# Kernel optimization log

Measured on AMD Instinct MI355X. Metric: run time of the kernel, lower is better.

Reference implementation:

```python
import jax, jax.numpy as jnp
import numpy as np

BONE_NUM = 16
THRESH = 0.7


def masked_l2(out, tar, mask):
    # out, tar: [B, C, H, W]; mask: [B, H, W]
    diff_norm = jnp.linalg.norm(out - tar, axis=1)          # [B, H, W]
    masked = jnp.where(mask > THRESH, diff_norm, 0.0)
    B = out.shape[0]
    flat_m = masked.reshape(B, -1)
    flat_d = diff_norm.reshape(B, -1)
    cnt = jnp.sum(flat_m != 0, axis=1)                       # device-side nonzero count
    per_sample = jnp.where(
        cnt > 0,
        flat_m.sum(axis=1) / jnp.maximum(cnt, 1).astype(flat_m.dtype),
        flat_d.mean(axis=1),
    )
    return per_sample.mean()


def pose_nocs_loss(pred_joint_map, pred_joint_score, out_mask, tar_joints):
    # pred_joint_map: [B, bn*3, H, W]; pred_joint_score: [B, bn, H, W]
    # out_mask: [B, H, W]; tar_joints: [B, bn, 3]
    B, _, H, W = pred_joint_map.shape
    bn = BONE_NUM
    jm = pred_joint_map.reshape(B, bn, 3, H, W) * out_mask[:, None, None]
    score = jax.nn.sigmoid(pred_joint_score) * out_mask[:, None]        # [B, bn, H, W]
    denom = score.reshape(B, bn, -1).sum(axis=2)[:, :, None, None] + 1e-5
    score_map = score / denom
    jm = jax.lax.stop_gradient(jm) * score_map[:, :, None]              # [B, bn, 3, H, W]
    pred_joint = jm.reshape(B, bn, 3, -1).sum(axis=3)                   # [B, bn, 3]
    loss = jnp.linalg.norm(pred_joint - tar_joints, axis=2).sum()
    return loss / (B * bn)


def setup_inputs() -> dict:
    key = jax.random.key(0)
    k1, k2, k3 = jax.random.split(key, 3)
    B, H, W = 4, 256, 256
    bn = BONE_NUM
    output = jax.random.normal(k1, (B, 4 + bn * 8 + 2, H, W), dtype=jnp.float32)
    tar_maps = jax.random.uniform(k2, (B, 4 + bn * 6 + 1, H, W), dtype=jnp.float32)
    tar_pose = jax.random.normal(k3, (B, bn, 6), dtype=jnp.float32)
    return {"output": output, "tar_maps": tar_maps, "tar_pose": tar_pose}


def reference(output, tar_maps, tar_pose):
    bn = BONE_NUM
    B = output.shape[0]

    # --- slice predictions ---
    pred_nocs = output[:, 0:3]
    mask_logits = output[:, 3]                                # sigmoid applied below
    pred_loc_map = jax.nn.sigmoid(output[:, 4:4 + bn * 3])
    pred_rot_map = jax.nn.sigmoid(output[:, 4 + bn * 3:4 + bn * 6])
    pred_skin_seg = output[:, 4 + bn * 6:4 + bn * 7 + 2]       # [B, bn+2, H, W]
    pred_joint_score = output[:, 4 + bn * 7 + 2:4 + bn * 8 + 2]  # [B, bn, H, W]

    # --- slice targets ---
    target_nocs = tar_maps[:, 0:3]
    target_mask = tar_maps[:, 3]
    tar_loc_map = jax.nn.sigmoid(tar_maps[:, 4:4 + bn * 3])
    tar_rot_map = jax.nn.sigmoid(tar_maps[:, 4 + bn * 3:4 + bn * 6])
    tar_skin_seg = tar_maps[:, 4 + bn * 6].astype(jnp.int32)   # [B, H, W]
    tar_loc = jax.nn.sigmoid(tar_pose[:, :, 0:3])
    tar_rot = jax.nn.sigmoid(tar_pose[:, :, 3:6])

    # --- BCE mask loss (on sigmoid(mask_logits) vs target_mask), stable form ---
    mask_loss = -jnp.mean(
        target_mask * jax.nn.log_sigmoid(mask_logits)
        + (1.0 - target_mask) * jax.nn.log_sigmoid(-mask_logits)
    )

    # --- masked L2 losses ---
    nocs_loss = masked_l2(pred_nocs, target_nocs, target_mask)
    loc_map_loss = masked_l2(pred_loc_map, tar_loc_map, target_mask)
    rot_map_loss = masked_l2(pred_rot_map, tar_rot_map, target_mask)

    # --- skinning cross entropy ---
    logits = jnp.transpose(pred_skin_seg, (0, 2, 3, 1)).reshape(-1, bn + 2)
    labels = tar_skin_seg.reshape(-1)
    logp = jax.nn.log_softmax(logits, axis=-1)
    skin_loss = -jnp.mean(jnp.take_along_axis(logp, labels[:, None], axis=1))

    # --- pose losses ---
    loc_loss = pose_nocs_loss(pred_loc_map, pred_joint_score, target_mask, tar_loc)
    rot_loss = pose_nocs_loss(pred_rot_map, pred_joint_score, target_mask, tar_rot)

    return jnp.stack([nocs_loss, mask_loss, loc_loss, loc_map_loss,
                      rot_loss, rot_map_loss, skin_loss])
```

## Files before the change

### kernel.cpp

```cpp
#include <hip/hip_runtime.h>
#include <math.h>

#define HW 65536
#define BN 16


__device__ __forceinline__ float fsig(float x) {
    return __builtin_amdgcn_rcpf(1.0f + __expf(-x));
}
__device__ __forceinline__ float sq(float x) { return x * x; }

__device__ __forceinline__ float wred(float v) {
#pragma unroll
    for (int off = 32; off; off >>= 1) v += __shfl_xor(v, off, 64);
    return v;
}

__global__ __launch_bounds__(256) void mvpm_pix2(const float* __restrict__ outp,
                                                 const float* __restrict__ tarp,
                                                 float* __restrict__ ws) {
    const int b = blockIdx.y;
    const int t = blockIdx.x * 256 + threadIdx.x;
    const int C2 = HW / 2;
    const float2* ob = (const float2*)(outp + (size_t)b * 134 * HW) + t;
    const float2* tb = (const float2*)(tarp + (size_t)b * 101 * HW) + t;
    const int lane = threadIdx.x & 63;
    const int wv = threadIdx.x >> 6;

    const float2 m2 = tb[3 * C2];
    const float2 ml = ob[3 * C2];
    const float2 a0 = ob[0], a1 = ob[C2], a2 = ob[2 * C2];
    const float2 b0 = tb[0], b1 = tb[C2], b2 = tb[2 * C2];

    const float bce =
        (m2.x * fminf(ml.x, 0.0f) + (1.0f - m2.x) * fminf(-ml.x, 0.0f)
         - __logf(1.0f + __expf(-fabsf(ml.x)))) +
        (m2.y * fminf(ml.y, 0.0f) + (1.0f - m2.y) * fminf(-ml.y, 0.0f)
         - __logf(1.0f + __expf(-fabsf(ml.y))));

    const float dnx = sqrtf(sq(a0.x - b0.x) + sq(a1.x - b1.x) + sq(a2.x - b2.x));
    const float dny = sqrtf(sq(a0.y - b0.y) + sq(a1.y - b1.y) + sq(a2.y - b2.y));
    const bool sx = m2.x > 0.7f, sy = m2.y > 0.7f;

    float2 x[18];
#pragma unroll
    for (int k = 0; k < 18; ++k) x[k] = ob[(100 + k) * C2];
    const float2 labf = tb[100 * C2];
    float mxx = x[0].x, mxy = x[0].y;
#pragma unroll
    for (int k = 1; k < 18; ++k) { mxx = fmaxf(mxx, x[k].x); mxy = fmaxf(mxy, x[k].y); }
    float sex = 0.0f, sey = 0.0f;
#pragma unroll
    for (int k = 0; k < 18; ++k) { sex += __expf(x[k].x - mxx); sey += __expf(x[k].y - mxy); }
    int labx = (int)labf.x; labx = labx < 0 ? 0 : (labx > 17 ? 17 : labx);
    int laby = (int)labf.y; laby = laby < 0 ? 0 : (laby > 17 ? 17 : laby);
    float xlx = x[0].x, xly = x[0].y;
#pragma unroll
    for (int k = 1; k < 18; ++k) { xlx = (labx == k) ? x[k].x : xlx;
                                   xly = (laby == k) ? x[k].y : xly; }
    const float skin = (mxx + __logf(sex) - xlx) + (mxy + __logf(sey) - xly);

    float dslx = 0.0f, dsly = 0.0f, dsrx = 0.0f, dsry = 0.0f;
#pragma unroll 2
    for (int j = 0; j < BN; ++j) {
        const int cl = (4 + 3 * j) * C2, cr = (52 + 3 * j) * C2;
        const float2 o0 = ob[cl], o1 = ob[cl + C2], o2 = ob[cl + 2 * C2];
        const float2 t0 = tb[cl], t1 = tb[cl + C2], t2 = tb[cl + 2 * C2];
        const float2 p0 = ob[cr], p1 = ob[cr + C2], p2 = ob[cr + 2 * C2];
        const float2 q0 = tb[cr], q1 = tb[cr + C2], q2 = tb[cr + 2 * C2];
        dslx += sq(fsig(o0.x) - fsig(t0.x)) + sq(fsig(o1.x) - fsig(t1.x))
              + sq(fsig(o2.x) - fsig(t2.x));
        dsly += sq(fsig(o0.y) - fsig(t0.y)) + sq(fsig(o1.y) - fsig(t1.y))
              + sq(fsig(o2.y) - fsig(t2.y));
        dsrx += sq(fsig(p0.x) - fsig(q0.x)) + sq(fsig(p1.x) - fsig(q1.x))
              + sq(fsig(p2.x) - fsig(q2.x));
        dsry += sq(fsig(p0.y) - fsig(q0.y)) + sq(fsig(p1.y) - fsig(q1.y))
              + sq(fsig(p2.y) - fsig(q2.y));
    }
    const float dnlx = sqrtf(dslx), dnly = sqrtf(dsly);
    const float dnrx = sqrtf(dsrx), dnry = sqrtf(dsry);

    float v[11];
    v[0]  = bce;
    v[1]  = skin;
    v[2]  = (sx ? dnx : 0.0f) + (sy ? dny : 0.0f);
    v[3]  = ((sx && dnx != 0.0f) ? 1.0f : 0.0f) + ((sy && dny != 0.0f) ? 1.0f : 0.0f);
    v[4]  = dnx + dny;
    v[5]  = (sx ? dnlx : 0.0f) + (sy ? dnly : 0.0f);
    v[6]  = ((sx && dnlx != 0.0f) ? 1.0f : 0.0f) + ((sy && dnly != 0.0f) ? 1.0f : 0.0f);
    v[7]  = dnlx + dnly;
    v[8]  = (sx ? dnrx : 0.0f) + (sy ? dnry : 0.0f);
    v[9]  = ((sx && dnrx != 0.0f) ? 1.0f : 0.0f) + ((sy && dnry != 0.0f) ? 1.0f : 0.0f);
    v[10] = dnrx + dnry;

#pragma unroll
    for (int off = 32; off; off >>= 1) {
#pragma unroll
        for (int i = 0; i < 11; ++i) v[i] += __shfl_xor(v[i], off, 64);
    }

    __shared__ float red[11][4];
    if (lane == 0) {
#pragma unroll
        for (int i = 0; i < 11; ++i) red[i][wv] = v[i];
    }
    __syncthreads();
    if (threadIdx.x < 11) {
        float s = red[threadIdx.x][0] + red[threadIdx.x][1] +
                  red[threadIdx.x][2] + red[threadIdx.x][3];
        int g = (threadIdx.x < 2) ? threadIdx.x : (2 + b * 9 + (threadIdx.x - 2));
        atomicAdd(&ws[g], s);
    }
}

__global__ __launch_bounds__(256) void mvpm_joint4(const float* __restrict__ outp,
                                                   const float* __restrict__ tarp,
                                                   float* __restrict__ ws) {
    const int bj = blockIdx.y;
    const int b = bj >> 4;
    const int j = bj & 15;
    const int C4 = HW / 4;
    const int idx = blockIdx.x * 256 + threadIdx.x;
    const float4* ob = (const float4*)(outp + (size_t)b * 134 * HW);
    const int lane = threadIdx.x & 63;
    const int wv = threadIdx.x >> 6;

    const float4 m  = ((const float4*)(tarp + (size_t)b * 101 * HW))[3 * C4 + idx];
    const float4 s  = ob[(118 + j) * C4 + idx];
    const float4 l0 = ob[(4 + 3 * j) * C4 + idx];
    const float4 l1 = ob[(5 + 3 * j) * C4 + idx];
    const float4 l2 = ob[(6 + 3 * j) * C4 + idx];
    const float4 r0 = ob[(52 + 3 * j) * C4 + idx];
    const float4 r1 = ob[(53 + 3 * j) * C4 + idx];
    const float4 r2 = ob[(54 + 3 * j) * C4 + idx];

    float wx = fsig(s.x) * m.x, wy = fsig(s.y) * m.y,
          wz = fsig(s.z) * m.z, ww = fsig(s.w) * m.w;
    float v[7];
    v[0] = wx + wy + wz + ww;
    wx *= m.x; wy *= m.y; wz *= m.z; ww *= m.w;
    v[1] = fsig(l0.x) * wx + fsig(l0.y) * wy + fsig(l0.z) * wz + fsig(l0.w) * ww;
    v[2] = fsig(l1.x) * wx + fsig(l1.y) * wy + fsig(l1.z) * wz + fsig(l1.w) * ww;
    v[3] = fsig(l2.x) * wx + fsig(l2.y) * wy + fsig(l2.z) * wz + fsig(l2.w) * ww;
    v[4] = fsig(r0.x) * wx + fsig(r0.y) * wy + fsig(r0.z) * wz + fsig(r0.w) * ww;
    v[5] = fsig(r1.x) * wx + fsig(r1.y) * wy + fsig(r1.z) * wz + fsig(r1.w) * ww;
    v[6] = fsig(r2.x) * wx + fsig(r2.y) * wy + fsig(r2.z) * wz + fsig(r2.w) * ww;

#pragma unroll
    for (int off = 32; off; off >>= 1) {
#pragma unroll
        for (int i = 0; i < 7; ++i) v[i] += __shfl_xor(v[i], off, 64);
    }

    __shared__ float red[7][4];
    if (lane == 0) {
#pragma unroll
        for (int i = 0; i < 7; ++i) red[i][wv] = v[i];
    }
    __syncthreads();
    if (threadIdx.x < 7) {
        float sum = red[threadIdx.x][0] + red[threadIdx.x][1] +
                    red[threadIdx.x][2] + red[threadIdx.x][3];
        atomicAdd(&ws[38 + bj * 7 + threadIdx.x], sum);
    }
}

__global__ __launch_bounds__(64) void mvpm_fin(const float* __restrict__ ws,
                                               const float* __restrict__ tp,
                                               float* __restrict__ o) {
    const int t = threadIdx.x;
    const int base = 38 + t * 7;

    float S = ws[base] + 1e-5f;
    float ln = 0.0f, rn = 0.0f;
#pragma unroll
    for (int c = 0; c < 3; ++c) {
        float pl = ws[base + 1 + c] / S;
        float tl = 1.0f / (1.0f + expf(-tp[t * 6 + c]));
        ln += (pl - tl) * (pl - tl);
        float pr = ws[base + 4 + c] / S;
        float tr = 1.0f / (1.0f + expf(-tp[t * 6 + 3 + c]));
        rn += (pr - tr) * (pr - tr);
    }
    ln = sqrtf(ln);
    rn = sqrtf(rn);
    float lsum = wred(ln);
    float rsum = wred(rn);

    if (t == 0) {
        float nocs = 0.0f, locm = 0.0f, rotm = 0.0f;
        for (int bb = 0; bb < 4; ++bb) {
            int ba = 2 + bb * 9;
            nocs += (ws[ba + 1] > 0.5f) ? ws[ba + 0] / ws[ba + 1] : ws[ba + 2] * (1.0f / HW);
            locm += (ws[ba + 4] > 0.5f) ? ws[ba + 3] / ws[ba + 4] : ws[ba + 5] * (1.0f / HW);
            rotm += (ws[ba + 7] > 0.5f) ? ws[ba + 6] / ws[ba + 7] : ws[ba + 8] * (1.0f / HW);
        }
        o[0] = nocs * 0.25f;
        o[1] = -ws[0] / (4.0f * HW);
        o[2] = lsum * (1.0f / 64.0f);
        o[3] = locm * 0.25f;
        o[4] = rsum * (1.0f / 64.0f);
        o[5] = rotm * 0.25f;
        o[6] = ws[1] / (4.0f * HW);
    }
}

extern "C" void kernel_launch(void* const* d_in, const int* in_sizes, int n_in,
                              void* d_out, int out_size, void* d_ws, size_t ws_size,
                              hipStream_t stream) {
    const float* outp = (const float*)d_in[0];
    const float* tarp = (const float*)d_in[1];
    const float* tpos = (const float*)d_in[2];
    float* o  = (float*)d_out;
    float* ws = (float*)d_ws;

    hipMemsetAsync(d_ws, 0, 486 * sizeof(float), stream);
    dim3 gA(HW / 512, 4);
    mvpm_pix2<<<gA, 256, 0, stream>>>(outp, tarp, ws);
    dim3 gB(HW / 1024, 64);
    mvpm_joint4<<<gB, 256, 0, stream>>>(outp, tarp, ws);
    mvpm_fin<<<1, 64, 0, stream>>>(ws, tpos, o);
}
```

Measured before the change: 290.9 us.

## Fuse joint-channel reads into one pass, storing per-joint squared-diff partials

```diff
diff --git a/kernel.cpp b/kernel.cpp
--- a/kernel.cpp
+++ b/kernel.cpp
@@ -3,6 +3,8 @@
 
 #define HW 65536
 #define BN 16
+#define QCH 16384
+#define PART_FLOATS 4194304
 
 
 __device__ __forceinline__ float fsig(float x) {
@@ -14,6 +16,191 @@
 #pragma unroll
     for (int off = 32; off; off >>= 1) v += __shfl_xor(v, off, 64);
     return v;
+}
+__device__ __forceinline__ float4 fsig4(float4 v) {
+    return make_float4(fsig(v.x), fsig(v.y), fsig(v.z), fsig(v.w));
+}
+__device__ __forceinline__ float dot4(float4 a, float4 b) {
+    return a.x * b.x + a.y * b.y + a.z * b.z + a.w * b.w;
+}
+__device__ __forceinline__ float4 sq3(float4 a0, float4 a1, float4 a2,
+                                      float4 b0, float4 b1, float4 b2) {
+    return make_float4(
+        sq(a0.x - b0.x) + sq(a1.x - b1.x) + sq(a2.x - b2.x),
+        sq(a0.y - b0.y) + sq(a1.y - b1.y) + sq(a2.y - b2.y),
+        sq(a0.z - b0.z) + sq(a1.z - b1.z) + sq(a2.z - b2.z),
+        sq(a0.w - b0.w) + sq(a1.w - b1.w) + sq(a2.w - b2.w));
+}
+
+__device__ __forceinline__ float skin_ce(const float* x, int lab) {
+    float mx = x[0];
+#pragma unroll
+    for (int k = 1; k < 18; ++k) mx = fmaxf(mx, x[k]);
+    float se = 0.0f;
+#pragma unroll
+    for (int k = 0; k < 18; ++k) se += __expf(x[k] - mx);
+    lab = lab < 0 ? 0 : (lab > 17 ? 17 : lab);
+    float xl = x[0];
+#pragma unroll
+    for (int k = 1; k < 18; ++k) xl = (lab == k) ? x[k] : xl;
+    return mx + __logf(se) - xl;
+}
+
+__global__ __launch_bounds__(256) void k1_joint(const float* __restrict__ outp,
+                                                const float* __restrict__ tarp,
+                                                float* __restrict__ ws) {
+    const int t = threadIdx.x;
+    const int slab = blockIdx.x;
+    const int b = blockIdx.y;
+    const int j = blockIdx.z;
+    const int lane = t & 63, wv = t >> 6;
+    const float4* ob = (const float4*)(outp + (size_t)b * 134 * HW);
+    const float4* tb = (const float4*)(tarp + (size_t)b * 101 * HW);
+    float4* dslp = ((float4*)(ws + 512)) + (size_t)(b * BN + j) * QCH;
+    float4* dsrp = ((float4*)(ws + 512 + PART_FLOATS)) + (size_t)(b * BN + j) * QCH;
+
+    const int cl = (4 + 3 * j) * QCH, cr = (52 + 3 * j) * QCH;
+    const int cs = (118 + j) * QCH, cm = 3 * QCH;
+
+    float S = 0.0f, NL0 = 0.0f, NL1 = 0.0f, NL2 = 0.0f,
+          NR0 = 0.0f, NR1 = 0.0f, NR2 = 0.0f;
+
+#pragma unroll 1
+    for (int k = 0; k < 4; ++k) {
+        const int q = slab * 1024 + k * 256 + t;
+        const float4 m  = tb[cm + q];
+        const float4 s  = ob[cs + q];
+        const float4 o0 = ob[cl + q];
+        const float4 o1 = ob[cl + QCH + q];
+        const float4 o2 = ob[cl + 2 * QCH + q];
+        const float4 t0 = tb[cl + q];
+        const float4 t1 = tb[cl + QCH + q];
+        const float4 t2 = tb[cl + 2 * QCH + q];
+        const float4 p0 = ob[cr + q];
+        const float4 p1 = ob[cr + QCH + q];
+        const float4 p2 = ob[cr + 2 * QCH + q];
+        const float4 u0 = tb[cr + q];
+        const float4 u1 = tb[cr + QCH + q];
+        const float4 u2 = tb[cr + 2 * QCH + q];
+
+        float4 w = fsig4(s);
+        w.x *= m.x; w.y *= m.y; w.z *= m.z; w.w *= m.w;
+        S += w.x + w.y + w.z + w.w;
+        float4 wm = w;
+        wm.x *= m.x; wm.y *= m.y; wm.z *= m.z; wm.w *= m.w;
+
+        const float4 so0 = fsig4(o0), so1 = fsig4(o1), so2 = fsig4(o2);
+        const float4 st0 = fsig4(t0), st1 = fsig4(t1), st2 = fsig4(t2);
+        const float4 sp0 = fsig4(p0), sp1 = fsig4(p1), sp2 = fsig4(p2);
+        const float4 su0 = fsig4(u0), su1 = fsig4(u1), su2 = fsig4(u2);
+
+        dslp[q] = sq3(so0, so1, so2, st0, st1, st2);
+        dsrp[q] = sq3(sp0, sp1, sp2, su0, su1, su2);
+
+        NL0 += dot4(so0, wm); NL1 += dot4(so1, wm); NL2 += dot4(so2, wm);
+        NR0 += dot4(sp0, wm); NR1 += dot4(sp1, wm); NR2 += dot4(sp2, wm);
+    }
+
+    float v[7] = {S, NL0, NL1, NL2, NR0, NR1, NR2};
+#pragma unroll
+    for (int off = 32; off; off >>= 1) {
+#pragma unroll
+        for (int i = 0; i < 7; ++i) v[i] += __shfl_xor(v[i], off, 64);
+    }
+    __shared__ float red[7][4];
+    if (lane == 0) {
+#pragma unroll
+        for (int i = 0; i < 7; ++i) red[i][wv] = v[i];
+    }
+    __syncthreads();
+    if (t < 7) {
+        float s = red[t][0] + red[t][1] + red[t][2] + red[t][3];
+        atomicAdd(&ws[38 + (b * BN + j) * 7 + t], s);
+    }
+}
+
+__global__ __launch_bounds__(256) void k2_pix(const float* __restrict__ outp,
+                                              const float* __restrict__ tarp,
+                                              float* __restrict__ ws) {
+    const int b = blockIdx.y;
+    const int q = blockIdx.x * 256 + threadIdx.x;
+    const int lane = threadIdx.x & 63, wv = threadIdx.x >> 6;
+    const float4* ob = (const float4*)(outp + (size_t)b * 134 * HW);
+    const float4* tb = (const float4*)(tarp + (size_t)b * 101 * HW);
+    const float4* dslp = ((const float4*)(ws + 512)) + (size_t)b * BN * QCH + q;
+    const float4* dsrp = ((const float4*)(ws + 512 + PART_FLOATS)) + (size_t)b * BN * QCH + q;
+
+    const float4 m  = tb[3 * QCH + q];
+    const float4 ml = ob[3 * QCH + q];
+    const float4 a0 = ob[q], a1 = ob[QCH + q], a2 = ob[2 * QCH + q];
+    const float4 b0 = tb[q], b1 = tb[QCH + q], b2 = tb[2 * QCH + q];
+    const float4 labf = tb[100 * QCH + q];
+
+    float x0[18], x1[18], x2[18], x3[18];
+#pragma unroll
+    for (int k = 0; k < 18; ++k) {
+        float4 xv = ob[(100 + k) * QCH + q];
+        x0[k] = xv.x; x1[k] = xv.y; x2[k] = xv.z; x3[k] = xv.w;
+    }
+
+    float4 dsl = make_float4(0.f, 0.f, 0.f, 0.f);
+    float4 dsr = make_float4(0.f, 0.f, 0.f, 0.f);
+#pragma unroll 4
+    for (int j = 0; j < BN; ++j) {
+        float4 a = dslp[(size_t)j * QCH];
+        float4 c = dsrp[(size_t)j * QCH];
+        dsl.x += a.x; dsl.y += a.y; dsl.z += a.z; dsl.w += a.w;
+        dsr.x += c.x; dsr.y += c.y; dsr.z += c.z; dsr.w += c.w;
+    }
+
+    float v[11];
+#pragma unroll
+    for (int i = 0; i < 11; ++i) v[i] = 0.0f;
+
+#define DO_COMP(C, XC)                                                         \
+    {                                                                          \
+        const float mc = m.C, mlc = ml.C;                                      \
+        v[0] += mc * fminf(mlc, 0.f) + (1.f - mc) * fminf(-mlc, 0.f)           \
+                - __logf(1.f + __expf(-fabsf(mlc)));                           \
+        v[1] += skin_ce(XC, (int)labf.C);                                      \
+        const float dn = sqrtf(sq(a0.C - b0.C) + sq(a1.C - b1.C) +             \
+                               sq(a2.C - b2.C));                               \
+        const bool sel = mc > 0.7f;                                            \
+        v[2] += sel ? dn : 0.f;                                                \
+        v[3] += (sel && dn != 0.f) ? 1.f : 0.f;                                \
+        v[4] += dn;                                                            \
+        const float dnl = sqrtf(dsl.C);                                        \
+        v[5] += sel ? dnl : 0.f;                                               \
+        v[6] += (sel && dnl != 0.f) ? 1.f : 0.f;                               \
+        v[7] += dnl;                                                           \
+        const float dnr = sqrtf(dsr.C);                                        \
+        v[8] += sel ? dnr : 0.f;                                               \
+        v[9] += (sel && dnr != 0.f) ? 1.f : 0.f;                               \
+        v[10] += dnr;                                                          \
+    }
+    DO_COMP(x, x0)
+    DO_COMP(y, x1)
+    DO_COMP(z, x2)
+    DO_COMP(w, x3)
+#undef DO_COMP
+
+#pragma unroll
+    for (int off = 32; off; off >>= 1) {
+#pragma unroll
+        for (int i = 0; i < 11; ++i) v[i] += __shfl_xor(v[i], off, 64);
+    }
+    __shared__ float red[11][4];
+    if (lane == 0) {
+#pragma unroll
+        for (int i = 0; i < 11; ++i) red[i][wv] = v[i];
+    }
+    __syncthreads();
+    if (threadIdx.x < 11) {
+        float s = red[threadIdx.x][0] + red[threadIdx.x][1] +
+                  red[threadIdx.x][2] + red[threadIdx.x][3];
+        int g = (threadIdx.x < 2) ? threadIdx.x : (2 + b * 9 + (threadIdx.x - 2));
+        atomicAdd(&ws[g], s);
+    }
 }
 
 __global__ __launch_bounds__(256) void mvpm_pix2(const float* __restrict__ outp,
@@ -42,23 +229,14 @@
     const float dny = sqrtf(sq(a0.y - b0.y) + sq(a1.y - b1.y) + sq(a2.y - b2.y));
     const bool sx = m2.x > 0.7f, sy = m2.y > 0.7f;
 
-    float2 x[18];
-#pragma unroll
-    for (int k = 0; k < 18; ++k) x[k] = ob[(100 + k) * C2];
+    float xx[18], xy[18];
+#pragma unroll
+    for (int k = 0; k < 18; ++k) {
+        float2 xv = ob[(100 + k) * C2];
+        xx[k] = xv.x; xy[k] = xv.y;
+    }
     const float2 labf = tb[100 * C2];
-    float mxx = x[0].x, mxy = x[0].y;
-#pragma unroll
-    for (int k = 1; k < 18; ++k) { mxx = fmaxf(mxx, x[k].x); mxy = fmaxf(mxy, x[k].y); }
-    float sex = 0.0f, sey = 0.0f;
-#pragma unroll
-    for (int k = 0; k < 18; ++k) { sex += __expf(x[k].x - mxx); sey += __expf(x[k].y - mxy); }
-    int labx = (int)labf.x; labx = labx < 0 ? 0 : (labx > 17 ? 17 : labx);
-    int laby = (int)labf.y; laby = laby < 0 ? 0 : (laby > 17 ? 17 : laby);
-    float xlx = x[0].x, xly = x[0].y;
-#pragma unroll
-    for (int k = 1; k < 18; ++k) { xlx = (labx == k) ? x[k].x : xlx;
-                                   xly = (laby == k) ? x[k].y : xly; }
-    const float skin = (mxx + __logf(sex) - xlx) + (mxy + __logf(sey) - xly);
+    const float skin = skin_ce(xx, (int)labf.x) + skin_ce(xy, (int)labf.y);
 
     float dslx = 0.0f, dsly = 0.0f, dsrx = 0.0f, dsry = 0.0f;
 #pragma unroll 2
@@ -98,7 +276,6 @@
 #pragma unroll
         for (int i = 0; i < 11; ++i) v[i] += __shfl_xor(v[i], off, 64);
     }
-
     __shared__ float red[11][4];
     if (lane == 0) {
 #pragma unroll
@@ -151,7 +328,6 @@
 #pragma unroll
         for (int i = 0; i < 7; ++i) v[i] += __shfl_xor(v[i], off, 64);
     }
-
     __shared__ float red[7][4];
     if (lane == 0) {
 #pragma unroll
@@ -215,9 +391,18 @@
     float* ws = (float*)d_ws;
 
     hipMemsetAsync(d_ws, 0, 486 * sizeof(float), stream);
-    dim3 gA(HW / 512, 4);
-    mvpm_pix2<<<gA, 256, 0, stream>>>(outp, tarp, ws);
-    dim3 gB(HW / 1024, 64);
-    mvpm_joint4<<<gB, 256, 0, stream>>>(outp, tarp, ws);
+
+    const size_t need = (size_t)(512 + 2 * PART_FLOATS) * sizeof(float);
+    if (ws_size >= need) {
+        dim3 g1(16, 4, 16);
+        k1_joint<<<g1, 256, 0, stream>>>(outp, tarp, ws);
+        dim3 g2(64, 4);
+        k2_pix<<<g2, 256, 0, stream>>>(outp, tarp, ws);
+    } else {
+        dim3 gA(HW / 512, 4);
+        mvpm_pix2<<<gA, 256, 0, stream>>>(outp, tarp, ws);
+        dim3 gB(HW / 1024, 64);
+        mvpm_joint4<<<gB, 256, 0, stream>>>(outp, tarp, ws);
+    }
     mvpm_fin<<<1, 64, 0, stream>>>(ws, tpos, o);
 }
```

New measurement: 304.3 us. 4.6% more time.
